# Kernel optimization log

Hardware: AMD Instinct MI355X
Metric: run time of the kernel (lower is better)

## Reference

```python
import jax, jax.numpy as jnp
import numpy as np

N_NODES = 50000
N_EDGES = 800000
D_IN = 128
D_HID = 512
D_OUT = 128


def setup_inputs() -> dict:
    key = jax.random.key(0)
    k1, k2, k3, k4, k5, k6 = jax.random.split(key, 6)
    input_matrix = jax.random.normal(k1, (N_NODES, D_IN), dtype=jnp.float32)
    adjacency_coo_matrix = jax.random.randint(k2, (2, N_EDGES), 0, N_NODES, dtype=jnp.int64)
    # fc net params (torch Linear: y = x @ W.T + b); store W already transposed [D_IN, D_HID]
    lim_fc = 1.0 / np.sqrt(D_IN)
    fc_w = jax.random.uniform(k3, (D_IN, D_HID), dtype=jnp.float32, minval=-lim_fc, maxval=lim_fc)
    fc_b = jax.random.uniform(k4, (D_HID,), dtype=jnp.float32, minval=-lim_fc, maxval=lim_fc)
    # xavier_uniform for [D_IN + D_HID, D_OUT]
    lim_w = np.sqrt(6.0 / (D_IN + D_HID + D_OUT))
    weights_matrix = jax.random.uniform(k5, (D_IN + D_HID, D_OUT), dtype=jnp.float32, minval=-lim_w, maxval=lim_w)
    return {
        "input_matrix": input_matrix,
        "fc_w": fc_w,
        "fc_b": fc_b,
        "weights_matrix": weights_matrix,
        "adjacency_coo_matrix": adjacency_coo_matrix,
    }


def reference(input_matrix, fc_w, fc_b, weights_matrix, adjacency_coo_matrix):
    edge_src, edge_trg = adjacency_coo_matrix[0], adjacency_coo_matrix[1]
    n_nodes = input_matrix.shape[0]
    # gather neighbor features: [E, D_IN]
    neighbors = input_matrix[edge_trg]
    # per-edge MLP + relu: [E, D_HID]
    neighbors_repr = jax.nn.relu(neighbors @ fc_w + fc_b)
    # scatter-max reduce into per-node slots; relu outputs are >= 0, and
    # empty segments map to 0 (matching torch_scatter zero-fill), so clamp at 0
    agg = jax.ops.segment_max(neighbors_repr, edge_src, num_segments=n_nodes)
    agg = jnp.maximum(agg, 0.0)
    concat = jnp.concatenate([input_matrix, agg], axis=1)  # [N, D_IN + D_HID]
    return concat @ weights_matrix  # [N, D_OUT]
```

## Files before the change

kernel.cpp:

```cpp
#include <hip/hip_runtime.h>
#include <hip/hip_bf16.h>

#define N_NODES 50000
#define N_EDGES 800000
#define D_IN 128
#define D_HID 512
#define D_OUT 128
#define CAT_DIM 640
#define CAP 64
#define CAPH 32
#define HALF 25000

typedef __attribute__((ext_vector_type(8))) short short8;
typedef __attribute__((ext_vector_type(4))) float floatx4;

__device__ __forceinline__ unsigned short f2bf(float f) {
    unsigned u = __float_as_uint(f);
    unsigned r = u + 0x7fffu + ((u >> 16) & 1u);
    return (unsigned short)(r >> 16);
}

__device__ __forceinline__ void cvt8(const float* __restrict__ src, unsigned short* o) {
    float4 v0 = *(const float4*)src;
    float4 v1 = *(const float4*)(src + 4);
    o[0] = f2bf(v0.x); o[1] = f2bf(v0.y); o[2] = f2bf(v0.z); o[3] = f2bf(v0.w);
    o[4] = f2bf(v1.x); o[5] = f2bf(v1.y); o[6] = f2bf(v1.z); o[7] = f2bf(v1.w);
}


#define NBKT 196
#define BKT_SHIFT 8
#define CAPB 6144
#define P1_CHUNK 4096
#define P1_BLOCKS 196


#define K0_FCW_BLOCKS 256
#define K0_WT_BLOCKS  320
#define K0_BLOCKS (K0_FCW_BLOCKS + K0_WT_BLOCKS + 1)

__global__ __launch_bounds__(256)
void prep_w_kernel(const float* __restrict__ fcW, const float* __restrict__ Wm,
                   unsigned short* __restrict__ fcwT, unsigned short* __restrict__ WT,
                   int* __restrict__ bucket_cnt) {
    int b = blockIdx.x, tid = threadIdx.x;
    if (b < K0_FCW_BLOCKS) {
        int idx = b * 256 + tid;
        int k = idx >> 9;
        int n = idx & (D_HID - 1);
        fcwT[n * D_IN + k] = f2bf(fcW[idx]);
        return;
    }
    b -= K0_FCW_BLOCKS;
    if (b < K0_WT_BLOCKS) {
        int idx = b * 256 + tid;
        int k = idx >> 7;
        int n = idx & (D_OUT - 1);
        WT[n * CAT_DIM + k] = f2bf(Wm[idx]);
        return;
    }
    if (tid < NBKT) bucket_cnt[tid] = 0;
}


#define S1_G1_BLOCKS 782
#define S1_BLOCKS (P1_BLOCKS + S1_G1_BLOCKS)
#define G1_PAD 8
#define SM1_BYTES (64 * (D_IN + G1_PAD) * 2 + 128 * (64 + G1_PAD) * 2)

__global__ __launch_bounds__(256)
void sort_gemm1_kernel(const int* __restrict__ adj,
                       int* __restrict__ bucket_cnt, uint2* __restrict__ staging,
                       const float* __restrict__ X,
                       const unsigned short* __restrict__ fcwT,
                       const float* __restrict__ fcb,
                       unsigned short* __restrict__ F) {
    __shared__ alignas(16) char smem[SM1_BYTES];
    int b = blockIdx.x, tid = threadIdx.x;
    if (b < P1_BLOCKS) {
        uint2* les = (uint2*)smem;
        int* cnt   = (int*)(smem + P1_CHUNK * 8);
        int* woff  = cnt + NBKT;
        for (int i = tid; i < NBKT; i += 256) cnt[i] = 0;
        int v = adj[2 * (tid & 63) + 1];
        int s = (__ballot(v != 0) == 0ULL) ? 2 : 1;
        __syncthreads();
        int e0 = b * P1_CHUNK;
        int ne = N_EDGES - e0; if (ne > P1_CHUNK) ne = P1_CHUNK;
        for (int j = tid; j < ne; j += 256) {
            int e = e0 + j;
            int src, trg;
            if (s == 2) { src = adj[2 * (size_t)e]; trg = adj[2 * ((size_t)N_EDGES + e)]; }
            else        { src = adj[e];             trg = adj[N_EDGES + e]; }
            les[j] = make_uint2((unsigned)src, (unsigned)trg);
            atomicAdd(&cnt[src >> BKT_SHIFT], 1);
        }
        __syncthreads();
        for (int i = tid; i < NBKT; i += 256)
            woff[i] = atomicAdd(&bucket_cnt[i], cnt[i]);
        __syncthreads();
        for (int j = tid; j < ne; j += 256) {
            uint2 et = les[j];
            int bk = (int)(et.x >> BKT_SHIFT);
            int pos = atomicAdd(&woff[bk], 1);
            if (pos < CAPB) staging[(size_t)bk * CAPB + pos] = et;
        }
        return;
    }
    b -= P1_BLOCKS;
    {
        typedef unsigned short RowA[D_IN + G1_PAD];
        typedef unsigned short RowB[64 + G1_PAD];
        RowA* As = (RowA*)smem;
        RowB* Bs = (RowB*)(smem + 64 * (D_IN + G1_PAD) * 2);
        int lane = tid & 63, w = tid >> 6;
        int bm = b * 64;
        {
            int r = tid >> 4;
            int c = (tid & 15) * 8;
            #pragma unroll
            for (int p = 0; p < 4; ++p) {
                int row = r + p * 16;
                int gr = bm + row;
                unsigned short o[8] = {0, 0, 0, 0, 0, 0, 0, 0};
                if (gr < N_NODES) cvt8(X + (size_t)gr * D_IN + c, o);
                *(uint4*)(&As[row][c]) = *(const uint4*)o;
            }
        }
        int wm = (w >> 1) * 32, wn = (w & 1) * 64;
        int q = lane >> 4, l16 = lane & 15;
        int rb = tid >> 1;
        int cb = (tid & 1) * 8;
        for (int nc = 0; nc < 4; ++nc) {
            floatx4 acc[2][4] = {};
            #pragma unroll
            for (int kh = 0; kh < 2; ++kh) {
                {
                    const unsigned short* bp = fcwT + (size_t)(nc * 128 + rb) * D_IN + kh * 64 + cb;
                    #pragma unroll
                    for (int p = 0; p < 4; ++p)
                        *(uint4*)(&Bs[rb][cb + p * 16]) = *(const uint4*)(bp + p * 16);
                }
                __syncthreads();
                #pragma unroll
                for (int ks = 0; ks < 2; ++ks) {
                    short8 af[2], bf[4];
                    #pragma unroll
                    for (int mi = 0; mi < 2; ++mi)
                        af[mi] = *(const short8*)(&As[wm + mi * 16 + l16][kh * 64 + ks * 32 + q * 8]);
                    #pragma unroll
                    for (int ni = 0; ni < 4; ++ni)
                        bf[ni] = *(const short8*)(&Bs[wn + ni * 16 + l16][ks * 32 + q * 8]);
                    #pragma unroll
                    for (int mi = 0; mi < 2; ++mi)
                        #pragma unroll
                        for (int ni = 0; ni < 4; ++ni)
                            acc[mi][ni] = __builtin_amdgcn_mfma_f32_16x16x32_bf16(af[mi], bf[ni], acc[mi][ni], 0, 0, 0);
                }
                __syncthreads();
            }
            #pragma unroll
            for (int mi = 0; mi < 2; ++mi)
                #pragma unroll
                for (int ni = 0; ni < 4; ++ni)
                    #pragma unroll
                    for (int r = 0; r < 4; ++r) {
                        int row = bm + wm + mi * 16 + q * 4 + r;
                        int col = nc * 128 + wn + ni * 16 + l16;
                        if (row < N_NODES) {
                            float v = fmaxf(acc[mi][ni][r] + fcb[col], 0.0f);
                            F[(size_t)row * D_HID + col] = f2bf(v);
                        }
                    }
        }
    }
}


__global__ __launch_bounds__(256)
void sort2_kernel(const int* __restrict__ bucket_cnt, const uint2* __restrict__ staging,
                  int* __restrict__ degp,
                  unsigned short* __restrict__ elLo, unsigned short* __restrict__ elHi) {
    __shared__ int lo[256], hi[256];
    int bk = blockIdx.x, tid = threadIdx.x;
    lo[tid] = 0; hi[tid] = 0;
    __syncthreads();
    int n = bucket_cnt[bk]; if (n > CAPB) n = CAPB;
    int base = bk << BKT_SHIFT;
    const uint2* st = staging + (size_t)bk * CAPB;
    for (int i = tid; i < n; i += 256) {
        uint2 et = st[i];
        int r = (int)et.x - base;
        int t = (int)et.y;
        if (t < HALF) {
            int p = atomicAdd(&lo[r], 1);
            if (p < CAPH) elLo[(size_t)(base + r) * CAPH + p] = (unsigned short)t;
        } else {
            int p = atomicAdd(&hi[r], 1);
            if (p < CAPH) elHi[(size_t)(base + r) * CAPH + p] = (unsigned short)t;
        }
    }
    __syncthreads();
    int src = base + tid;
    if (src < N_NODES) degp[src] = lo[tid] | (hi[tid] << 16);
}


__device__ __forceinline__ void fmax_bf16x8(float* acc, const uint4& p) {
    const unsigned* a = (const unsigned*)&p;
    #pragma unroll
    for (int j = 0; j < 4; ++j) {
        unsigned u = a[j];
        acc[2 * j]     = fmaxf(acc[2 * j],     __uint_as_float(u << 16));
        acc[2 * j + 1] = fmaxf(acc[2 * j + 1], __uint_as_float(u & 0xffff0000u));
    }
}

#define AGG_CHUNKS 1563

template<int H>
__global__ __launch_bounds__(256)
void aggregate_phase(const unsigned short* __restrict__ F,
                     const int* __restrict__ degp,
                     const unsigned short* __restrict__ el,
                     unsigned short* __restrict__ agg) {
    int tid = threadIdx.x;
    int s = blockIdx.x & 7;
    int chunk = blockIdx.x >> 3;
    int n = chunk * 32 + (tid >> 3);
    int ch = tid & 7;
    if (n >= N_NODES) return;
    int dp = degp[n];
    int d = H ? (dp >> 16) : (dp & 0xffff);
    d = d < CAPH ? d : CAPH;
    const unsigned short* Fs = F + s * 64 + ch * 8;
    const unsigned short* ep = el + (size_t)n * CAPH;
    unsigned short* ap = agg + (size_t)n * D_HID + s * 64 + ch * 8;
    float acc[8];
    if (H) {
        uint4 a0 = *(const uint4*)ap;
        const unsigned* au = (const unsigned*)&a0;
        #pragma unroll
        for (int j = 0; j < 4; ++j) {
            acc[2 * j]     = __uint_as_float(au[j] << 16);
            acc[2 * j + 1] = __uint_as_float(au[j] & 0xffff0000u);
        }
    } else {
        #pragma unroll
        for (int j = 0; j < 8; ++j) acc[j] = 0.0f;
    }
    #pragma unroll 2
    for (int i = 0; i < d; ++i) {
        int t = ep[i];
        uint4 p = *(const uint4*)(Fs + (size_t)t * D_HID);
        fmax_bf16x8(acc, p);
    }
    unsigned o[4];
    #pragma unroll
    for (int j = 0; j < 4; ++j) {
        unsigned lov = __float_as_uint(acc[2 * j]) >> 16;
        unsigned hiv = __float_as_uint(acc[2 * j + 1]) & 0xffff0000u;
        o[j] = lov | hiv;
    }
    *(uint4*)ap = *(uint4*)o;
}


#define GPAD 8
#define GEMM_MT 782

__global__ __launch_bounds__(256)
void gemm2_kernel(const float* __restrict__ X,
                  const unsigned short* __restrict__ agg,
                  const unsigned short* __restrict__ WT,
                  float* __restrict__ out) {
    __shared__ unsigned short As[64][64 + GPAD];
    __shared__ unsigned short Bs[128][64 + GPAD];
    int tid = threadIdx.x;
    int lane = tid & 63, w = tid >> 6;
    int wm = (w >> 1) * 32, wn = (w & 1) * 64;
    int q = lane >> 4, l16 = lane & 15;
    int bm = blockIdx.x * 64;
    floatx4 acc[2][4] = {};
    int ra = tid >> 2;
    int ca = (tid & 3) * 8;
    int rb = tid >> 1;
    int cb = (tid & 1) * 8;

    for (int k0 = 0; k0 < CAT_DIM; k0 += 64) {
        {
            int gr = bm + ra;
            #pragma unroll
            for (int p = 0; p < 2; ++p) {
                int col = k0 + ca + p * 32;
                unsigned short o[8] = {0, 0, 0, 0, 0, 0, 0, 0};
                if (gr < N_NODES) {
                    if (col < D_IN) cvt8(X + (size_t)gr * D_IN + col, o);
                    else *(uint4*)o = *(const uint4*)(agg + (size_t)gr * D_HID + (col - D_IN));
                }
                *(uint4*)(&As[ra][ca + p * 32]) = *(const uint4*)o;
            }
        }
        {
            const unsigned short* bp = WT + (size_t)rb * CAT_DIM + k0 + cb;
            #pragma unroll
            for (int p = 0; p < 4; ++p)
                *(uint4*)(&Bs[rb][cb + p * 16]) = *(const uint4*)(bp + p * 16);
        }
        __syncthreads();
        #pragma unroll
        for (int ks = 0; ks < 2; ++ks) {
            short8 af[2], bf[4];
            #pragma unroll
            for (int mi = 0; mi < 2; ++mi)
                af[mi] = *(const short8*)(&As[wm + mi * 16 + l16][ks * 32 + q * 8]);
            #pragma unroll
            for (int ni = 0; ni < 4; ++ni)
                bf[ni] = *(const short8*)(&Bs[wn + ni * 16 + l16][ks * 32 + q * 8]);
            #pragma unroll
            for (int mi = 0; mi < 2; ++mi)
                #pragma unroll
                for (int ni = 0; ni < 4; ++ni)
                    acc[mi][ni] = __builtin_amdgcn_mfma_f32_16x16x32_bf16(af[mi], bf[ni], acc[mi][ni], 0, 0, 0);
        }
        __syncthreads();
    }

    #pragma unroll
    for (int mi = 0; mi < 2; ++mi)
        #pragma unroll
        for (int ni = 0; ni < 4; ++ni)
            #pragma unroll
            for (int r = 0; r < 4; ++r) {
                int row = bm + wm + mi * 16 + q * 4 + r;
                int col = wn + ni * 16 + l16;
                if (row < N_NODES)
                    out[(size_t)row * D_OUT + col] = acc[mi][ni][r];
            }
}


extern "C" void kernel_launch(void* const* d_in, const int* in_sizes, int n_in,
                              void* d_out, int out_size, void* d_ws, size_t ws_size,
                              hipStream_t stream) {
    const float* X    = (const float*)d_in[0];
    const float* fc_w = (const float*)d_in[1];
    const float* fc_b = (const float*)d_in[2];
    const float* Wm   = (const float*)d_in[3];
    const int*   adj  = (const int*)d_in[4];
    float* outp = (float*)d_out;

    char* ws = (char*)d_ws;
    size_t off = 0;
    auto alloc = [&](size_t bytes) -> void* {
        void* p = ws + off;
        off = (off + bytes + 255) & ~(size_t)255;
        return p;
    };
    unsigned short* agg    = (unsigned short*)alloc((size_t)N_NODES * D_HID * 2);
    unsigned short* F      = (unsigned short*)alloc((size_t)N_NODES * D_HID * 2);
    unsigned short* fcwT   = (unsigned short*)alloc((size_t)D_HID * D_IN * 2);
    unsigned short* WT     = (unsigned short*)alloc((size_t)D_OUT * CAT_DIM * 2);
    int* degp      = (int*)alloc((size_t)N_NODES * 4);
    unsigned short* elLo = (unsigned short*)alloc((size_t)N_NODES * CAPH * 2);
    unsigned short* elHi = (unsigned short*)alloc((size_t)N_NODES * CAPH * 2);
    int* bucket_cnt = (int*)alloc((size_t)NBKT * 4);
    uint2* staging  = (uint2*)alloc((size_t)NBKT * CAPB * 8);

    prep_w_kernel<<<K0_BLOCKS, 256, 0, stream>>>(fc_w, Wm, fcwT, WT, bucket_cnt);
    sort_gemm1_kernel<<<S1_BLOCKS, 256, 0, stream>>>(adj, bucket_cnt, staging,
                                                     X, fcwT, fc_b, F);
    sort2_kernel<<<NBKT, 256, 0, stream>>>(bucket_cnt, staging, degp, elLo, elHi);
    aggregate_phase<0><<<AGG_CHUNKS * 8, 256, 0, stream>>>(F, degp, elLo, agg);
    aggregate_phase<1><<<AGG_CHUNKS * 8, 256, 0, stream>>>(F, degp, elHi, agg);
    gemm2_kernel<<<GEMM_MT, 256, 0, stream>>>(X, agg, WT, outp);
}
```

Measured before the change: 250.4 us.

## Merge two aggregation phases into one launch with separate partial max buffers

New measurement: 249.4 us. Within noise of the previous version (-0.4%).

```diff
diff --git a/kernel.cpp b/kernel.cpp
--- a/kernel.cpp
+++ b/kernel.cpp
@@ -7,7 +7,6 @@
 #define D_HID 512
 #define D_OUT 128
 #define CAT_DIM 640
-#define CAP 64
 #define CAPH 32
 #define HALF 25000
 
@@ -74,7 +73,8 @@
                        const float* __restrict__ X,
                        const unsigned short* __restrict__ fcwT,
                        const float* __restrict__ fcb,
-                       unsigned short* __restrict__ F) {
+                       unsigned short* __restrict__ F,
+                       unsigned short* __restrict__ Xb) {
     __shared__ alignas(16) char smem[SM1_BYTES];
     int b = blockIdx.x, tid = threadIdx.x;
     if (b < P1_BLOCKS) {
@@ -123,7 +123,10 @@
                 int row = r + p * 16;
                 int gr = bm + row;
                 unsigned short o[8] = {0, 0, 0, 0, 0, 0, 0, 0};
-                if (gr < N_NODES) cvt8(X + (size_t)gr * D_IN + c, o);
+                if (gr < N_NODES) {
+                    cvt8(X + (size_t)gr * D_IN + c, o);
+                    *(uint4*)(Xb + (size_t)gr * D_IN + c) = *(const uint4*)o;
+                }
                 *(uint4*)(&As[row][c]) = *(const uint4*)o;
             }
         }
@@ -217,38 +220,33 @@
 }
 
 #define AGG_CHUNKS 1563
-
-template<int H>
-__global__ __launch_bounds__(256)
-void aggregate_phase(const unsigned short* __restrict__ F,
-                     const int* __restrict__ degp,
-                     const unsigned short* __restrict__ el,
-                     unsigned short* __restrict__ agg) {
+#define AGG_PHASE_BLOCKS (AGG_CHUNKS * 8)
+
+__global__ __launch_bounds__(256)
+void aggregate_all_kernel(const unsigned short* __restrict__ F,
+                          const int* __restrict__ degp,
+                          const unsigned short* __restrict__ elLo,
+                          const unsigned short* __restrict__ elHi,
+                          unsigned short* __restrict__ aggLo,
+                          unsigned short* __restrict__ aggHi) {
     int tid = threadIdx.x;
-    int s = blockIdx.x & 7;
-    int chunk = blockIdx.x >> 3;
+    int H = blockIdx.x >= AGG_PHASE_BLOCKS;
+    int pb = blockIdx.x - H * AGG_PHASE_BLOCKS;
+    int s = pb & 7;
+    int chunk = pb >> 3;
     int n = chunk * 32 + (tid >> 3);
     int ch = tid & 7;
     if (n >= N_NODES) return;
     int dp = degp[n];
     int d = H ? (dp >> 16) : (dp & 0xffff);
     d = d < CAPH ? d : CAPH;
+    const unsigned short* el = H ? elHi : elLo;
+    unsigned short* agg = H ? aggHi : aggLo;
     const unsigned short* Fs = F + s * 64 + ch * 8;
     const unsigned short* ep = el + (size_t)n * CAPH;
-    unsigned short* ap = agg + (size_t)n * D_HID + s * 64 + ch * 8;
     float acc[8];
-    if (H) {
-        uint4 a0 = *(const uint4*)ap;
-        const unsigned* au = (const unsigned*)&a0;
-        #pragma unroll
-        for (int j = 0; j < 4; ++j) {
-            acc[2 * j]     = __uint_as_float(au[j] << 16);
-            acc[2 * j + 1] = __uint_as_float(au[j] & 0xffff0000u);
-        }
-    } else {
-        #pragma unroll
-        for (int j = 0; j < 8; ++j) acc[j] = 0.0f;
-    }
+    #pragma unroll
+    for (int j = 0; j < 8; ++j) acc[j] = 0.0f;
     #pragma unroll 2
     for (int i = 0; i < d; ++i) {
         int t = ep[i];
@@ -262,7 +260,7 @@
         unsigned hiv = __float_as_uint(acc[2 * j + 1]) & 0xffff0000u;
         o[j] = lov | hiv;
     }
-    *(uint4*)ap = *(uint4*)o;
+    *(uint4*)(agg + (size_t)n * D_HID + s * 64 + ch * 8) = *(uint4*)o;
 }
 
 
@@ -270,8 +268,9 @@
 #define GEMM_MT 782
 
 __global__ __launch_bounds__(256)
-void gemm2_kernel(const float* __restrict__ X,
-                  const unsigned short* __restrict__ agg,
+void gemm2_kernel(const unsigned short* __restrict__ Xb,
+                  const unsigned short* __restrict__ aggLo,
+                  const unsigned short* __restrict__ aggHi,
                   const unsigned short* __restrict__ WT,
                   float* __restrict__ out) {
     __shared__ unsigned short As[64][64 + GPAD];
@@ -295,8 +294,17 @@
                 int col = k0 + ca + p * 32;
                 unsigned short o[8] = {0, 0, 0, 0, 0, 0, 0, 0};
                 if (gr < N_NODES) {
-                    if (col < D_IN) cvt8(X + (size_t)gr * D_IN + col, o);
-                    else *(uint4*)o = *(const uint4*)(agg + (size_t)gr * D_HID + (col - D_IN));
+                    if (col < D_IN) {
+                        *(uint4*)o = *(const uint4*)(Xb + (size_t)gr * D_IN + col);
+                    } else {
+                        uint4 vl = *(const uint4*)(aggLo + (size_t)gr * D_HID + (col - D_IN));
+                        uint4 vh = *(const uint4*)(aggHi + (size_t)gr * D_HID + (col - D_IN));
+                        const unsigned short* pl = (const unsigned short*)&vl;
+                        const unsigned short* ph = (const unsigned short*)&vh;
+                        #pragma unroll
+                        for (int j = 0; j < 8; ++j)
+                            o[j] = pl[j] > ph[j] ? pl[j] : ph[j];
+                    }
                 }
                 *(uint4*)(&As[ra][ca + p * 32]) = *(const uint4*)o;
             }
@@ -357,8 +365,10 @@
         off = (off + bytes + 255) & ~(size_t)255;
         return p;
     };
-    unsigned short* agg    = (unsigned short*)alloc((size_t)N_NODES * D_HID * 2);
+    unsigned short* aggLo  = (unsigned short*)alloc((size_t)N_NODES * D_HID * 2);
+    unsigned short* aggHi  = (unsigned short*)alloc((size_t)N_NODES * D_HID * 2);
     unsigned short* F      = (unsigned short*)alloc((size_t)N_NODES * D_HID * 2);
+    unsigned short* Xb     = (unsigned short*)alloc((size_t)N_NODES * D_IN * 2);
     unsigned short* fcwT   = (unsigned short*)alloc((size_t)D_HID * D_IN * 2);
     unsigned short* WT     = (unsigned short*)alloc((size_t)D_OUT * CAT_DIM * 2);
     int* degp      = (int*)alloc((size_t)N_NODES * 4);
@@ -369,9 +379,9 @@
 
     prep_w_kernel<<<K0_BLOCKS, 256, 0, stream>>>(fc_w, Wm, fcwT, WT, bucket_cnt);
     sort_gemm1_kernel<<<S1_BLOCKS, 256, 0, stream>>>(adj, bucket_cnt, staging,
-                                                     X, fcwT, fc_b, F);
+                                                     X, fcwT, fc_b, F, Xb);
     sort2_kernel<<<NBKT, 256, 0, stream>>>(bucket_cnt, staging, degp, elLo, elHi);
-    aggregate_phase<0><<<AGG_CHUNKS * 8, 256, 0, stream>>>(F, degp, elLo, agg);
-    aggregate_phase<1><<<AGG_CHUNKS * 8, 256, 0, stream>>>(F, degp, elHi, agg);
-    gemm2_kernel<<<GEMM_MT, 256, 0, stream>>>(X, agg, WT, outp);
-}
+    aggregate_all_kernel<<<AGG_PHASE_BLOCKS * 2, 256, 0, stream>>>(F, degp, elLo, elHi,
+                                                                   aggLo, aggHi);
+    gemm2_kernel<<<GEMM_MT, 256, 0, stream>>>(Xb, aggLo, aggHi, WT, outp);
+}
```
